# Optimization experiments

Hardware: AMD Instinct MI355X
Metric: run time of the kernel (lower is better)

## Reference

```python
import jax, jax.numpy as jnp
import numpy as np

B = 4096          # number of sampled constraints (batch)
H = 1024          # hidden_size
N_UNIT = 5
MAXD = 4          # max(DEPTHS)
TAU = 1.0
N_STEPS = N_UNIT * (1 + 2 * MAXD)  # 45
CLIST = np.linspace(10.0, 20.0, 5).astype(np.float32)
NSC = 11
DEPTH_VALS = np.array([2, 3, 4])
RATIO_VALS = np.array([3, 4, 6])
KS_VALS = np.array([3, 5, 7])


def setup_inputs() -> dict:
    key = jax.random.key(0)
    ks = jax.random.split(key, 20)
    def p(k, shape):
        return jax.random.uniform(k, shape, minval=-0.1, maxval=0.1, dtype=jnp.float32)
    return {
        'constraints': jax.random.uniform(ks[0], (B,), minval=10.0, maxval=20.0, dtype=jnp.float32),
        'superclass_id': 3,
        'gumbel_u': jax.random.uniform(ks[1], (N_STEPS, B, 3), minval=1e-6, maxval=1.0 - 1e-6, dtype=jnp.float32),
        'cond_emb': p(ks[2], (len(CLIST), H // 2)),
        'sc_emb': p(ks[3], (NSC, H // 2)),
        'depth_emb': p(ks[4], (3, H)),
        'ratio_emb': p(ks[5], (3, H)),
        'ks_emb': p(ks[6], (3, H)),
        'W_ih': p(ks[7], (4 * H, H)), 'b_ih': p(ks[8], (4 * H,)),
        'W_hh': p(ks[9], (4 * H, H)), 'b_hh': p(ks[10], (4 * H,)),
        'depth_W': p(ks[11], (3, H)), 'depth_b': p(ks[12], (3,)),
        'width_W': p(ks[13], (3, H)), 'width_b': p(ks[14], (3,)),
        'ks_W': p(ks[15], (3, H)), 'ks_b': p(ks[16], (3,)),
    }


def reference(constraints, superclass_id, gumbel_u, cond_emb, sc_emb, depth_emb, ratio_emb,
              ks_emb, W_ih, b_ih, W_hh, b_hh, depth_W, depth_b, width_W, width_b, ks_W, ks_b):
    clist = jnp.asarray(CLIST)
    # linear_interpolation: find bracketing interval for each constraint
    idx = jnp.clip(jnp.searchsorted(clist, constraints, side='right') - 1, 0, clist.shape[0] - 2)
    left, right = clist[idx], clist[idx + 1]
    w = ((right - constraints) / (right - left))[:, None]
    cemb = w * cond_emb[idx] + (1.0 - w) * cond_emb[idx + 1]          # [B, H/2]
    sce = jnp.broadcast_to(sc_emb[superclass_id], (constraints.shape[0], sc_emb.shape[1]))
    embed = jnp.concatenate([cemb, sce], axis=1)                       # [B, H]
    h = jnp.zeros((constraints.shape[0], H), embed.dtype)
    c = h

    def lstm(x, h, c):
        gates = x @ W_ih.T + b_ih + h @ W_hh.T + b_hh                  # [B, 4H]
        i, f, g, o = jnp.split(gates, 4, axis=-1)
        c2 = jax.nn.sigmoid(f) * c + jax.nn.sigmoid(i) * jnp.tanh(g)
        h2 = jax.nn.sigmoid(o) * jnp.tanh(c2)
        return h2, c2

    def gsample(logits, u):
        g = -jnp.log(-jnp.log(u))
        y_soft = jax.nn.softmax((logits + g) / TAU, axis=-1)
        onehot = jax.nn.one_hot(jnp.argmax(y_soft, -1), logits.shape[-1], dtype=y_soft.dtype)
        y_hard = onehot - jax.lax.stop_gradient(y_soft) + y_soft       # straight-through
        return jnp.argmax(y_hard, -1), y_soft, y_hard

    t = 0
    d_idx, d_probs, d_wbs = [], [], []
    r_idx, r_probs, r_wbs = [], [], []
    k_idx, k_probs, k_wbs = [], [], []
    for _unit in range(N_UNIT):
        h, c = lstm(embed, h, c)
        s, ys, yh = gsample(h @ depth_W.T + depth_b, gumbel_u[t]); t += 1
        d_idx.append(s); d_probs.append(ys); d_wbs.append(yh)
        embed = depth_emb[s]
        for _blk in range(MAXD):
            h, c = lstm(embed, h, c)
            s, ys, yh = gsample(h @ width_W.T + width_b, gumbel_u[t]); t += 1
            r_idx.append(s); r_probs.append(ys); r_wbs.append(yh)
            embed = ratio_emb[s]
            h, c = lstm(embed, h, c)
            s, ys, yh = gsample(h @ ks_W.T + ks_b, gumbel_u[t]); t += 1
            k_idx.append(s); k_probs.append(ys); k_wbs.append(yh)
            embed = ks_emb[s]

    depths = jnp.asarray(DEPTH_VALS)[jnp.stack(d_idx)]   # [5, B]
    ratios = jnp.asarray(RATIO_VALS)[jnp.stack(r_idx)]   # [20, B]
    kss = jnp.asarray(KS_VALS)[jnp.stack(k_idx)]         # [20, B]
    return (depths, ratios, kss,
            jnp.stack(d_wbs), jnp.stack(d_probs),
            jnp.stack(r_wbs), jnp.stack(r_probs),
            jnp.stack(k_wbs), jnp.stack(k_probs))
```

## Files before the change

### kernel.cpp

```cpp
#include <hip/hip_runtime.h>
#include <cmath>

namespace {

typedef _Float16 f16;
typedef f16 f16x8 __attribute__((ext_vector_type(8)));
typedef f16 f16x4 __attribute__((ext_vector_type(4)));
typedef float f32x4 __attribute__((ext_vector_type(4)));

constexpr int B  = 4096;
constexpr int H  = 1024;
constexpr int FH = 4 * H;
constexpr int NSTEPS = 45;
constexpr float INVS = 1.0f / 2048.0f;

__device__ __forceinline__ float sigf(float x) { return 1.0f / (1.0f + expf(-x)); }

struct HL { f16 h, l; };
__device__ __forceinline__ HL split16(float a) {
  float ah = (float)(f16)a;
  if (fabsf(a) < 6.1035156e-5f) ah = 0.0f;
  HL r; r.h = (f16)ah; r.l = (f16)((a - ah) * 2048.0f); return r;
}

__device__ __forceinline__ void async16(f16* lds_dst, const f16* gsrc) {
  __builtin_amdgcn_global_load_lds(
      (const __attribute__((address_space(1))) void*)gsrc,
      (__attribute__((address_space(3))) void*)lds_dst, 16, 0, 0);
}

__global__ void packW_kernel(const float* __restrict__ W, f16* __restrict__ packed) {
  int tid  = blockIdx.x * 256 + threadIdx.x;
  int lane = tid & 63;
  int rest = tid >> 6;
  int hl = rest & 1;
  int nf = (rest >> 1) & 3;
  int wn = (rest >> 3) & 1;
  int kt = (rest >> 4) & 31;
  int jb = rest >> 9;
  int row = nf * 1024 + jb * 32 + wn * 16 + (lane & 15);
  int kk  = kt * 32 + (lane >> 4) * 8;
  const float* src = W + (size_t)row * H + kk;
  f16x8 v;
  #pragma unroll
  for (int i = 0; i < 8; ++i) {
    HL s = split16(src[i]);
    v[i] = hl ? s.l : s.h;
  }
  *(f16x8*)(packed + (size_t)tid * 8) = v;
}

__global__ void precompute_kernel(
    const float* __restrict__ W_ih, const float* __restrict__ b_ih, const float* __restrict__ b_hh,
    const float* __restrict__ depth_emb, const float* __restrict__ ratio_emb, const float* __restrict__ ks_emb,
    const float* __restrict__ cond_emb, const float* __restrict__ sc_emb, const int* __restrict__ sid_p,
    float* __restrict__ tblD, float* __restrict__ tblR, float* __restrict__ tblK,
    float* __restrict__ condp, float* __restrict__ base0) {
  const int w4   = threadIdx.x >> 6;
  const int lane = threadIdx.x & 63;
  const int j    = blockIdx.x * 4 + w4;
  const float* wr = W_ih + (size_t)j * H;
  const int k = lane * 16;
  float4 wv0 = *(const float4*)(wr + k);
  float4 wv1 = *(const float4*)(wr + k + 4);
  float4 wv2 = *(const float4*)(wr + k + 8);
  float4 wv3 = *(const float4*)(wr + k + 12);

  auto dot = [&](const float* e) -> float {
    float4 e0 = *(const float4*)(e);
    float4 e1 = *(const float4*)(e + 4);
    float4 e2 = *(const float4*)(e + 8);
    float4 e3 = *(const float4*)(e + 12);
    return e0.x*wv0.x + e0.y*wv0.y + e0.z*wv0.z + e0.w*wv0.w
         + e1.x*wv1.x + e1.y*wv1.y + e1.z*wv1.z + e1.w*wv1.w
         + e2.x*wv2.x + e2.y*wv2.y + e2.z*wv2.z + e2.w*wv2.w
         + e3.x*wv3.x + e3.y*wv3.y + e3.z*wv3.z + e3.w*wv3.w;
  };

  float a[15];
  a[0] = dot(depth_emb + k);       a[1] = dot(depth_emb + H + k);   a[2] = dot(depth_emb + 2*H + k);
  a[3] = dot(ratio_emb + k);       a[4] = dot(ratio_emb + H + k);   a[5] = dot(ratio_emb + 2*H + k);
  a[6] = dot(ks_emb + k);          a[7] = dot(ks_emb + H + k);      a[8] = dot(ks_emb + 2*H + k);
  a[9] = a[10] = a[11] = a[12] = a[13] = a[14] = 0.0f;
  constexpr int HH = H / 2;
  int sid = sid_p[0];
  if (lane < 32) {
    a[9]  = dot(cond_emb + 0*HH + k);
    a[10] = dot(cond_emb + 1*HH + k);
    a[11] = dot(cond_emb + 2*HH + k);
    a[12] = dot(cond_emb + 3*HH + k);
    a[13] = dot(cond_emb + 4*HH + k);
  } else {
    a[14] = dot(sc_emb + sid*HH + (k - HH));
  }
  #pragma unroll
  for (int i = 0; i < 15; ++i) {
    #pragma unroll
    for (int off = 32; off > 0; off >>= 1) a[i] += __shfl_xor(a[i], off);
  }
  if (lane == 0) {
    float bias = b_ih[j] + b_hh[j];
    tblD[0*FH+j]=a[0]+bias; tblD[1*FH+j]=a[1]+bias; tblD[2*FH+j]=a[2]+bias;
    tblR[0*FH+j]=a[3]+bias; tblR[1*FH+j]=a[4]+bias; tblR[2*FH+j]=a[5]+bias;
    tblK[0*FH+j]=a[6]+bias; tblK[1*FH+j]=a[7]+bias; tblK[2*FH+j]=a[8]+bias;
    condp[0*FH+j]=a[9]; condp[1*FH+j]=a[10]; condp[2*FH+j]=a[11];
    condp[3*FH+j]=a[12]; condp[4*FH+j]=a[13];
    base0[j] = a[14] + bias;
  }
}

__global__ void step0_kernel(const float* __restrict__ constraints,
                             const float* __restrict__ condp, const float* __restrict__ base0,
                             f16* __restrict__ hhi, f16* __restrict__ hlo, float* __restrict__ c) {
  int idx = blockIdx.x * blockDim.x + threadIdx.x;
  int b = idx >> 10;
  int j = idx & (H - 1);
  float cv = constraints[b];
  int i0 = 0;
  if (cv >= 12.5f) i0 = 1;
  if (cv >= 15.0f) i0 = 2;
  if (cv >= 17.5f) i0 = 3;
  float right = 10.0f + 2.5f * (float)(i0 + 1);
  float w = (right - cv) / 2.5f;
  const float* c0 = condp + (size_t)i0 * FH;
  const float* c1 = c0 + FH;
  float iw = 1.0f - w;
  float xi = w*c0[j]       + iw*c1[j]       + base0[j];
  float xg = w*c0[2*H+j]   + iw*c1[2*H+j]   + base0[2*H+j];
  float xo = w*c0[3*H+j]   + iw*c1[3*H+j]   + base0[3*H+j];
  float cn = sigf(xi) * tanhf(xg);
  float hn = sigf(xo) * tanhf(cn);
  c[idx] = cn;
  HL s = split16(hn);
  hhi[idx] = s.h; hlo[idx] = s.l;
}

constexpr int ABUF = 16384;

__global__ __launch_bounds__(512, 2) void lstm_step_mfma(
    const f16* __restrict__ hhi, const f16* __restrict__ hlo,
    f16* __restrict__ nhhi, f16* __restrict__ nhlo,
    float* __restrict__ cbuf,
    const f16* __restrict__ packW,
    const float* __restrict__ tbl, const int* __restrict__ sel) {
  __shared__ __align__(16) f16 lds[3 * ABUF];

  const int tid  = threadIdx.x;
  const int lane = tid & 63;
  const int w    = tid >> 6;
  const int wm   = w >> 1, wn = w & 1;
  const int l15  = lane & 15;
  const int kq   = lane >> 4;

  const int L   = blockIdx.x;
  const int xcd = L & 7, seq = L >> 3;
  const int jb  = (xcd << 2) + (seq & 3);
  const int bb  = seq >> 2;
  const int b0  = bb << 8;
  const int j0  = jb << 5;

  f32x4 accH[4][4] = {};
  f32x4 accL[4][4] = {};

  int offA[4];
  #pragma unroll
  for (int mf = 0; mf < 4; ++mf) {
    int R = wm * 64 + mf * 16 + l15;
    int c = kq ^ (R & 3) ^ ((R >> 2) & 3);
    offA[mf] = R * 32 + c * 8;
  }

  const int rs = tid >> 2, cs = tid & 3;
  const int r1 = 128 + rs;
  const int cl0 = cs ^ (rs & 3) ^ ((rs >> 2) & 3);
  const int cl1 = cs ^ (r1 & 3) ^ ((r1 >> 2) & 3);
  const f16* sA0h = hhi + (size_t)(b0 + rs) * H + cl0 * 8;
  const f16* sA0l = hlo + (size_t)(b0 + rs) * H + cl0 * 8;
  const f16* sA1h = hhi + (size_t)(b0 + r1) * H + cl1 * 8;
  const f16* sA1l = hlo + (size_t)(b0 + r1) * H + cl1 * 8;
  const int dA0 = w * 512, dA1 = 4096 + w * 512;

  f16 *bA = lds, *bB = lds + ABUF, *bC = lds + 2 * ABUF;

  auto stageA = [&](f16* buf, int ko) {
    async16(buf + dA0,        sA0h + ko);
    async16(buf + dA0 + 8192, sA0l + ko);
    async16(buf + dA1,        sA1h + ko);
    async16(buf + dA1 + 8192, sA1l + ko);
  };

  const f16* wb = packW + (size_t)jb * 262144 + wn * 4096 + lane * 8;

  f16x8 bh0[4], bh1[4], bl[4];

  stageA(bA, 0);
  stageA(bB, 32);
  #pragma unroll
  for (int nf = 0; nf < 4; ++nf) bh0[nf] = *(const f16x8*)(wb + nf * 1024);
  asm volatile("s_waitcnt vmcnt(8)" ::: "memory");
  __builtin_amdgcn_s_barrier();

  auto tile = [&](int kt, f16x8 (&bhC)[4], f16x8 (&bhN)[4]) {
    const f16* wt = wb + (size_t)kt * 8192;
    #pragma unroll
    for (int nf = 0; nf < 4; ++nf) bl[nf] = *(const f16x8*)(wt + nf * 1024 + 512);
    if (kt < 30) stageA(bC, (kt + 2) * 32);
    if (kt < 31) {
      #pragma unroll
      for (int nf = 0; nf < 4; ++nf) bhN[nf] = *(const f16x8*)(wt + 8192 + nf * 1024);
    }
    f16x8 ah[4], al[4];
    #pragma unroll
    for (int mf = 0; mf < 4; ++mf) {
      ah[mf] = *(const f16x8*)(bA + offA[mf]);
      al[mf] = *(const f16x8*)(bA + offA[mf] + 8192);
    }
    #pragma unroll
    for (int mf = 0; mf < 4; ++mf)
      #pragma unroll
      for (int nf = 0; nf < 4; ++nf)
        accH[mf][nf] = __builtin_amdgcn_mfma_f32_16x16x32_f16(ah[mf], bhC[nf], accH[mf][nf], 0, 0, 0);
    #pragma unroll
    for (int mf = 0; mf < 4; ++mf)
      #pragma unroll
      for (int nf = 0; nf < 4; ++nf) {
        accL[mf][nf] = __builtin_amdgcn_mfma_f32_16x16x32_f16(ah[mf], bl[nf], accL[mf][nf], 0, 0, 0);
        accL[mf][nf] = __builtin_amdgcn_mfma_f32_16x16x32_f16(al[mf], bhC[nf], accL[mf][nf], 0, 0, 0);
      }
    __builtin_amdgcn_s_barrier();
    f16* tt = bA; bA = bB; bB = bC; bC = tt;
  };

  for (int kt = 0; kt < 32; kt += 2) {
    tile(kt,     bh0, bh1);
    tile(kt + 1, bh1, bh0);
  }

  const int j = j0 + wn * 16 + l15;
  #pragma unroll
  for (int mf = 0; mf < 4; ++mf) {
    #pragma unroll
    for (int r = 0; r < 4; ++r) {
      int b = b0 + wm * 64 + mf * 16 + kq * 4 + r;
      int s = sel[b];
      const float* tb = tbl + (size_t)s * FH + j;
      float gi = accH[mf][0][r] + accL[mf][0][r] * INVS + tb[0];
      float gf = accH[mf][1][r] + accL[mf][1][r] * INVS + tb[H];
      float gg = accH[mf][2][r] + accL[mf][2][r] * INVS + tb[2*H];
      float go = accH[mf][3][r] + accL[mf][3][r] * INVS + tb[3*H];
      size_t off = (size_t)b * H + j;
      float cp = cbuf[off];
      float cn = sigf(gf) * cp + sigf(gi) * tanhf(gg);
      float hn = sigf(go) * tanhf(cn);
      cbuf[off] = cn;
      HL sp = split16(hn);
      nhhi[off] = sp.h;
      nhlo[off] = sp.l;
    }
  }
}

__global__ void sampler_kernel(const f16* __restrict__ hhi, const f16* __restrict__ hlo,
                               const float* __restrict__ selW, const float* __restrict__ selb,
                               const float* __restrict__ gu,
                               float* __restrict__ val_out, float* __restrict__ wb_out,
                               float* __restrict__ p_out,
                               float v0, float v1, float v2,
                               int* __restrict__ sel) {
  int wave = threadIdx.x >> 6;
  int lane = threadIdx.x & 63;
  int b = blockIdx.x * 4 + wave;
  const f16* hh = hhi + (size_t)b * H;
  const f16* hl = hlo + (size_t)b * H;
  float acc0 = 0, acc1 = 0, acc2 = 0;
  #pragma unroll
  for (int ch = 0; ch < 4; ++ch) {
    int k = ch * 256 + lane * 4;
    f16x4 vh = *(const f16x4*)(hh + k);
    f16x4 vl = *(const f16x4*)(hl + k);
    float x0 = (float)vh[0] + (float)vl[0] * INVS;
    float x1 = (float)vh[1] + (float)vl[1] * INVS;
    float x2 = (float)vh[2] + (float)vl[2] * INVS;
    float x3 = (float)vh[3] + (float)vl[3] * INVS;
    float4 w0 = *(const float4*)(selW + k);
    float4 w1 = *(const float4*)(selW + H + k);
    float4 w2 = *(const float4*)(selW + 2*H + k);
    acc0 += x0*w0.x + x1*w0.y + x2*w0.z + x3*w0.w;
    acc1 += x0*w1.x + x1*w1.y + x2*w1.z + x3*w1.w;
    acc2 += x0*w2.x + x1*w2.y + x2*w2.z + x3*w2.w;
  }
  #pragma unroll
  for (int off = 32; off > 0; off >>= 1) {
    acc0 += __shfl_xor(acc0, off);
    acc1 += __shfl_xor(acc1, off);
    acc2 += __shfl_xor(acc2, off);
  }
  if (lane == 0) {
    float y0 = acc0 + selb[0] - logf(-logf(gu[(size_t)b*3 + 0]));
    float y1 = acc1 + selb[1] - logf(-logf(gu[(size_t)b*3 + 1]));
    float y2 = acc2 + selb[2] - logf(-logf(gu[(size_t)b*3 + 2]));
    int s = 0;
    float best = y0;
    if (y1 > best) { s = 1; best = y1; }
    if (y2 > best) { s = 2; best = y2; }
    float e0 = expf(y0 - best), e1 = expf(y1 - best), e2 = expf(y2 - best);
    float inv = 1.0f / (e0 + e1 + e2);
    float p0 = e0 * inv, p1 = e1 * inv, p2 = e2 * inv;
    val_out[b] = (s == 0) ? v0 : ((s == 1) ? v1 : v2);
    wb_out[(size_t)b*3 + 0] = (s == 0) ? 1.0f : 0.0f;
    wb_out[(size_t)b*3 + 1] = (s == 1) ? 1.0f : 0.0f;
    wb_out[(size_t)b*3 + 2] = (s == 2) ? 1.0f : 0.0f;
    p_out[(size_t)b*3 + 0] = p0;
    p_out[(size_t)b*3 + 1] = p1;
    p_out[(size_t)b*3 + 2] = p2;
    sel[b] = s;
  }
}

}

extern "C" void kernel_launch(void* const* d_in, const int* in_sizes, int n_in,
                              void* d_out, int out_size, void* d_ws, size_t ws_size,
                              hipStream_t stream) {
  (void)in_sizes; (void)n_in; (void)out_size; (void)ws_size;
  const float* constraints = (const float*)d_in[0];
  const int*   sid         = (const int*)d_in[1];
  const float* gumbel      = (const float*)d_in[2];
  const float* cond_emb    = (const float*)d_in[3];
  const float* sc_emb      = (const float*)d_in[4];
  const float* depth_emb   = (const float*)d_in[5];
  const float* ratio_emb   = (const float*)d_in[6];
  const float* ks_emb      = (const float*)d_in[7];
  const float* W_ih        = (const float*)d_in[8];
  const float* b_ih        = (const float*)d_in[9];
  const float* W_hh        = (const float*)d_in[10];
  const float* b_hh        = (const float*)d_in[11];
  const float* depth_W     = (const float*)d_in[12];
  const float* depth_b     = (const float*)d_in[13];
  const float* width_W     = (const float*)d_in[14];
  const float* width_b     = (const float*)d_in[15];
  const float* ks_W        = (const float*)d_in[16];
  const float* ks_b        = (const float*)d_in[17];

  float* out = (float*)d_out;
  float* ws  = (float*)d_ws;

  float* cb    = ws;
  f16*   packW = (f16*)(cb + (size_t)B * H);
  f16*   hhiA  = packW + (size_t)8 * 1024 * 1024;
  f16*   hloA  = hhiA + (size_t)B * H;
  f16*   hhiB  = hloA + (size_t)B * H;
  f16*   hloB  = hhiB + (size_t)B * H;
  float* tblD  = (float*)(hloB + (size_t)B * H);
  float* tblR  = tblD + 3 * FH;
  float* tblK  = tblR + 3 * FH;
  float* condp = tblK + 3 * FH;
  float* base0 = condp + 5 * FH;
  int*   sel   = (int*)(base0 + FH);

  packW_kernel<<<4096, 256, 0, stream>>>(W_hh, packW);
  precompute_kernel<<<FH / 4, 256, 0, stream>>>(
      W_ih, b_ih, b_hh, depth_emb, ratio_emb, ks_emb, cond_emb, sc_emb, sid,
      tblD, tblR, tblK, condp, base0);
  step0_kernel<<<(B * H) / 256, 256, 0, stream>>>(constraints, condp, base0, hhiA, hloA, cb);

  const float* selW_arr[3] = {depth_W, width_W, ks_W};
  const float* selb_arr[3] = {depth_b, width_b, ks_b};
  const float vals[3][3]   = {{2.f,3.f,4.f},{3.f,4.f,6.f},{3.f,5.f,7.f}};
  float* tbl_arr[3]        = {tblD, tblR, tblK};

  const size_t DEPTHS = 0,            RATIOS = (size_t)5*B,   KSS    = (size_t)25*B,
               DWBS   = (size_t)45*B, DPROBS = (size_t)60*B,
               RWBS   = (size_t)75*B, RPROBS = (size_t)135*B,
               KWBS   = (size_t)195*B, KPROBS = (size_t)255*B;

  f16* hhi_cur = hhiA; f16* hlo_cur = hloA;
  f16* hhi_nxt = hhiB; f16* hlo_nxt = hloB;
  for (int t = 0; t < NSTEPS; ++t) {
    if (t > 0) {
      int pt = (t - 1) % 9;
      int ptype = (pt == 0) ? 0 : ((pt & 1) ? 1 : 2);
      lstm_step_mfma<<<512, 512, 0, stream>>>(
          hhi_cur, hlo_cur, hhi_nxt, hlo_nxt, cb, packW, tbl_arr[ptype], sel);
      f16* th = hhi_cur; hhi_cur = hhi_nxt; hhi_nxt = th;
      f16* tl = hlo_cur; hlo_cur = hlo_nxt; hlo_nxt = tl;
    }
    int r = t % 9, u = t / 9;
    int ty, row;
    float *valp, *wbp, *pp;
    if (r == 0)      { ty = 0; row = u;
      valp = out + DEPTHS + (size_t)row*B; wbp = out + DWBS + (size_t)row*B*3; pp = out + DPROBS + (size_t)row*B*3; }
    else if (r & 1)  { ty = 1; row = u*4 + (r-1)/2;
      valp = out + RATIOS + (size_t)row*B; wbp = out + RWBS + (size_t)row*B*3; pp = out + RPROBS + (size_t)row*B*3; }
    else             { ty = 2; row = u*4 + (r-2)/2;
      valp = out + KSS + (size_t)row*B;    wbp = out + KWBS + (size_t)row*B*3; pp = out + KPROBS + (size_t)row*B*3; }
    sampler_kernel<<<B / 4, 256, 0, stream>>>(
        hhi_cur, hlo_cur, selW_arr[ty], selb_arr[ty], gumbel + (size_t)t * B * 3,
        valp, wbp, pp, vals[ty][0], vals[ty][1], vals[ty][2], sel);
  }
}
```

Before: 5.705 ms.

## Store hidden state in MFMA-fragment packed layout and load A directly from global

The hi/lo split hidden state now lives in one buffer laid out in MFMA A-fragment order. The LSTM step kernel drops its LDS triple-buffered async staging and barriers, and each wave reads its A fragments straight from global memory (mostly L2) while double-buffering the W fragments in registers. The step0 kernel, the step epilogue and the sampler are changed to write and read this packed layout. Launch bounds move to one block per CU, which trades occupancy for register room, and every wave now refetches A from global with no LDS reuse across the two column waves.

```diff
diff --git a/kernel.cpp b/kernel.cpp
--- a/kernel.cpp
+++ b/kernel.cpp
@@ -23,11 +23,6 @@
   HL r; r.h = (f16)ah; r.l = (f16)((a - ah) * 2048.0f); return r;
 }
 
-__device__ __forceinline__ void async16(f16* lds_dst, const f16* gsrc) {
-  __builtin_amdgcn_global_load_lds(
-      (const __attribute__((address_space(1))) void*)gsrc,
-      (__attribute__((address_space(3))) void*)lds_dst, 16, 0, 0);
-}
 
 __global__ void packW_kernel(const float* __restrict__ W, f16* __restrict__ packed) {
   int tid  = blockIdx.x * 256 + threadIdx.x;
@@ -111,7 +106,7 @@
 
 __global__ void step0_kernel(const float* __restrict__ constraints,
                              const float* __restrict__ condp, const float* __restrict__ base0,
-                             f16* __restrict__ hhi, f16* __restrict__ hlo, float* __restrict__ c) {
+                             f16* __restrict__ hpack, float* __restrict__ c) {
   int idx = blockIdx.x * blockDim.x + threadIdx.x;
   int b = idx >> 10;
   int j = idx & (H - 1);
@@ -132,19 +127,17 @@
   float hn = sigf(xo) * tanhf(cn);
   c[idx] = cn;
   HL s = split16(hn);
-  hhi[idx] = s.h; hlo[idx] = s.l;
-}
-
-constexpr int ABUF = 16384;
-
-__global__ __launch_bounds__(512, 2) void lstm_step_mfma(
-    const f16* __restrict__ hhi, const f16* __restrict__ hlo,
-    f16* __restrict__ nhhi, f16* __restrict__ nhlo,
+  size_t u = (size_t)((b >> 4) * 32 + (j >> 5));
+  int off = ((b & 15) + 16 * ((j >> 3) & 3)) * 8 + (j & 7);
+  hpack[u * 1024 + off]       = s.h;
+  hpack[u * 1024 + off + 512] = s.l;
+}
+
+__global__ __launch_bounds__(512, 1) void lstm_step_mfma(
+    const f16* __restrict__ hpack, f16* __restrict__ npack,
     float* __restrict__ cbuf,
     const f16* __restrict__ packW,
     const float* __restrict__ tbl, const int* __restrict__ sel) {
-  __shared__ __align__(16) f16 lds[3 * ABUF];
-
   const int tid  = threadIdx.x;
   const int lane = tid & 63;
   const int w    = tid >> 6;
@@ -162,58 +155,35 @@
   f32x4 accH[4][4] = {};
   f32x4 accL[4][4] = {};
 
-  int offA[4];
-  #pragma unroll
-  for (int mf = 0; mf < 4; ++mf) {
-    int R = wm * 64 + mf * 16 + l15;
-    int c = kq ^ (R & 3) ^ ((R >> 2) & 3);
-    offA[mf] = R * 32 + c * 8;
-  }
-
-  const int rs = tid >> 2, cs = tid & 3;
-  const int r1 = 128 + rs;
-  const int cl0 = cs ^ (rs & 3) ^ ((rs >> 2) & 3);
-  const int cl1 = cs ^ (r1 & 3) ^ ((r1 >> 2) & 3);
-  const f16* sA0h = hhi + (size_t)(b0 + rs) * H + cl0 * 8;
-  const f16* sA0l = hlo + (size_t)(b0 + rs) * H + cl0 * 8;
-  const f16* sA1h = hhi + (size_t)(b0 + r1) * H + cl1 * 8;
-  const f16* sA1l = hlo + (size_t)(b0 + r1) * H + cl1 * 8;
-  const int dA0 = w * 512, dA1 = 4096 + w * 512;
-
-  f16 *bA = lds, *bB = lds + ABUF, *bC = lds + 2 * ABUF;
-
-  auto stageA = [&](f16* buf, int ko) {
-    async16(buf + dA0,        sA0h + ko);
-    async16(buf + dA0 + 8192, sA0l + ko);
-    async16(buf + dA1,        sA1h + ko);
-    async16(buf + dA1 + 8192, sA1l + ko);
-  };
+  const f16* abase[4];
+  #pragma unroll
+  for (int mf = 0; mf < 4; ++mf)
+    abase[mf] = hpack + ((size_t)((b0 >> 4) + wm * 4 + mf) * 32) * 1024 + lane * 8;
 
   const f16* wb = packW + (size_t)jb * 262144 + wn * 4096 + lane * 8;
 
-  f16x8 bh0[4], bh1[4], bl[4];
-
-  stageA(bA, 0);
-  stageA(bB, 32);
-  #pragma unroll
-  for (int nf = 0; nf < 4; ++nf) bh0[nf] = *(const f16x8*)(wb + nf * 1024);
-  asm volatile("s_waitcnt vmcnt(8)" ::: "memory");
-  __builtin_amdgcn_s_barrier();
-
-  auto tile = [&](int kt, f16x8 (&bhC)[4], f16x8 (&bhN)[4]) {
-    const f16* wt = wb + (size_t)kt * 8192;
-    #pragma unroll
-    for (int nf = 0; nf < 4; ++nf) bl[nf] = *(const f16x8*)(wt + nf * 1024 + 512);
-    if (kt < 30) stageA(bC, (kt + 2) * 32);
+  f16x8 bhX[4], blX[4], bhY[4], blY[4];
+
+  #pragma unroll
+  for (int nf = 0; nf < 4; ++nf) {
+    bhX[nf] = *(const f16x8*)(wb + nf * 1024);
+    blX[nf] = *(const f16x8*)(wb + nf * 1024 + 512);
+  }
+
+  auto tile = [&](int kt, f16x8 (&bhC)[4], f16x8 (&blC)[4],
+                          f16x8 (&bhN)[4], f16x8 (&blN)[4]) {
+    f16x8 ah[4], al[4];
+    #pragma unroll
+    for (int mf = 0; mf < 4; ++mf) ah[mf] = *(const f16x8*)(abase[mf] + kt * 1024);
+    #pragma unroll
+    for (int mf = 0; mf < 4; ++mf) al[mf] = *(const f16x8*)(abase[mf] + kt * 1024 + 512);
     if (kt < 31) {
+      const f16* wt = wb + (size_t)(kt + 1) * 8192;
       #pragma unroll
-      for (int nf = 0; nf < 4; ++nf) bhN[nf] = *(const f16x8*)(wt + 8192 + nf * 1024);
-    }
-    f16x8 ah[4], al[4];
-    #pragma unroll
-    for (int mf = 0; mf < 4; ++mf) {
-      ah[mf] = *(const f16x8*)(bA + offA[mf]);
-      al[mf] = *(const f16x8*)(bA + offA[mf] + 8192);
+      for (int nf = 0; nf < 4; ++nf) {
+        bhN[nf] = *(const f16x8*)(wt + nf * 1024);
+        blN[nf] = *(const f16x8*)(wt + nf * 1024 + 512);
+      }
     }
     #pragma unroll
     for (int mf = 0; mf < 4; ++mf)
@@ -223,22 +193,25 @@
     #pragma unroll
     for (int mf = 0; mf < 4; ++mf)
       #pragma unroll
-      for (int nf = 0; nf < 4; ++nf) {
-        accL[mf][nf] = __builtin_amdgcn_mfma_f32_16x16x32_f16(ah[mf], bl[nf], accL[mf][nf], 0, 0, 0);
+      for (int nf = 0; nf < 4; ++nf)
+        accL[mf][nf] = __builtin_amdgcn_mfma_f32_16x16x32_f16(ah[mf], blC[nf], accL[mf][nf], 0, 0, 0);
+    #pragma unroll
+    for (int mf = 0; mf < 4; ++mf)
+      #pragma unroll
+      for (int nf = 0; nf < 4; ++nf)
         accL[mf][nf] = __builtin_amdgcn_mfma_f32_16x16x32_f16(al[mf], bhC[nf], accL[mf][nf], 0, 0, 0);
-      }
-    __builtin_amdgcn_s_barrier();
-    f16* tt = bA; bA = bB; bB = bC; bC = tt;
   };
 
   for (int kt = 0; kt < 32; kt += 2) {
-    tile(kt,     bh0, bh1);
-    tile(kt + 1, bh1, bh0);
+    tile(kt,     bhX, blX, bhY, blY);
+    tile(kt + 1, bhY, blY, bhX, blX);
   }
 
   const int j = j0 + wn * 16 + l15;
+  const int eoff = (wn * 2 + (l15 >> 3)) * 128 + (l15 & 7);
   #pragma unroll
   for (int mf = 0; mf < 4; ++mf) {
+    const size_t ubase = ((size_t)((b0 >> 4) + wm * 4 + mf) * 32 + jb) * 1024;
     #pragma unroll
     for (int r = 0; r < 4; ++r) {
       int b = b0 + wm * 64 + mf * 16 + kq * 4 + r;
@@ -254,13 +227,14 @@
       float hn = sigf(go) * tanhf(cn);
       cbuf[off] = cn;
       HL sp = split16(hn);
-      nhhi[off] = sp.h;
-      nhlo[off] = sp.l;
+      size_t pa = ubase + (size_t)((kq * 4 + r) * 8 + eoff);
+      npack[pa]       = sp.h;
+      npack[pa + 512] = sp.l;
     }
   }
 }
 
-__global__ void sampler_kernel(const f16* __restrict__ hhi, const f16* __restrict__ hlo,
+__global__ void sampler_kernel(const f16* __restrict__ hpack,
                                const float* __restrict__ selW, const float* __restrict__ selb,
                                const float* __restrict__ gu,
                                float* __restrict__ val_out, float* __restrict__ wb_out,
@@ -270,24 +244,25 @@
   int wave = threadIdx.x >> 6;
   int lane = threadIdx.x & 63;
   int b = blockIdx.x * 4 + wave;
-  const f16* hh = hhi + (size_t)b * H;
-  const f16* hl = hlo + (size_t)b * H;
+  const f16* hp = hpack + ((size_t)(b >> 4) * 32) * 1024 + (b & 15) * 8;
   float acc0 = 0, acc1 = 0, acc2 = 0;
   #pragma unroll
-  for (int ch = 0; ch < 4; ++ch) {
-    int k = ch * 256 + lane * 4;
-    f16x4 vh = *(const f16x4*)(hh + k);
-    f16x4 vl = *(const f16x4*)(hl + k);
-    float x0 = (float)vh[0] + (float)vl[0] * INVS;
-    float x1 = (float)vh[1] + (float)vl[1] * INVS;
-    float x2 = (float)vh[2] + (float)vl[2] * INVS;
-    float x3 = (float)vh[3] + (float)vl[3] * INVS;
-    float4 w0 = *(const float4*)(selW + k);
-    float4 w1 = *(const float4*)(selW + H + k);
-    float4 w2 = *(const float4*)(selW + 2*H + k);
-    acc0 += x0*w0.x + x1*w0.y + x2*w0.z + x3*w0.w;
-    acc1 += x0*w1.x + x1*w1.y + x2*w1.z + x3*w1.w;
-    acc2 += x0*w2.x + x1*w2.y + x2*w2.z + x3*w2.w;
+  for (int c2 = 0; c2 < 2; ++c2) {
+    int c = lane + c2 * 64;
+    const f16* base = hp + (c >> 2) * 1024 + (c & 3) * 128;
+    f16x8 vh = *(const f16x8*)(base);
+    f16x8 vl = *(const f16x8*)(base + 512);
+    int j = c * 8;
+    const float* w0p = selW + j;
+    const float* w1p = selW + H + j;
+    const float* w2p = selW + 2 * H + j;
+    #pragma unroll
+    for (int i = 0; i < 8; ++i) {
+      float x = (float)vh[i] + (float)vl[i] * INVS;
+      acc0 += x * w0p[i];
+      acc1 += x * w1p[i];
+      acc2 += x * w2p[i];
+    }
   }
   #pragma unroll
   for (int off = 32; off > 0; off >>= 1) {
@@ -347,11 +322,9 @@
 
   float* cb    = ws;
   f16*   packW = (f16*)(cb + (size_t)B * H);
-  f16*   hhiA  = packW + (size_t)8 * 1024 * 1024;
-  f16*   hloA  = hhiA + (size_t)B * H;
-  f16*   hhiB  = hloA + (size_t)B * H;
-  f16*   hloB  = hhiB + (size_t)B * H;
-  float* tblD  = (float*)(hloB + (size_t)B * H);
+  f16*   hpkA  = packW + (size_t)8 * 1024 * 1024;
+  f16*   hpkB  = hpkA + (size_t)B * H * 2;
+  float* tblD  = (float*)(hpkB + (size_t)B * H * 2);
   float* tblR  = tblD + 3 * FH;
   float* tblK  = tblR + 3 * FH;
   float* condp = tblK + 3 * FH;
@@ -362,7 +335,7 @@
   precompute_kernel<<<FH / 4, 256, 0, stream>>>(
       W_ih, b_ih, b_hh, depth_emb, ratio_emb, ks_emb, cond_emb, sc_emb, sid,
       tblD, tblR, tblK, condp, base0);
-  step0_kernel<<<(B * H) / 256, 256, 0, stream>>>(constraints, condp, base0, hhiA, hloA, cb);
+  step0_kernel<<<(B * H) / 256, 256, 0, stream>>>(constraints, condp, base0, hpkA, cb);
 
   const float* selW_arr[3] = {depth_W, width_W, ks_W};
   const float* selb_arr[3] = {depth_b, width_b, ks_b};
@@ -374,16 +347,15 @@
                RWBS   = (size_t)75*B, RPROBS = (size_t)135*B,
                KWBS   = (size_t)195*B, KPROBS = (size_t)255*B;
 
-  f16* hhi_cur = hhiA; f16* hlo_cur = hloA;
-  f16* hhi_nxt = hhiB; f16* hlo_nxt = hloB;
+  f16* hcur = hpkA;
+  f16* hnxt = hpkB;
   for (int t = 0; t < NSTEPS; ++t) {
     if (t > 0) {
       int pt = (t - 1) % 9;
       int ptype = (pt == 0) ? 0 : ((pt & 1) ? 1 : 2);
       lstm_step_mfma<<<512, 512, 0, stream>>>(
-          hhi_cur, hlo_cur, hhi_nxt, hlo_nxt, cb, packW, tbl_arr[ptype], sel);
-      f16* th = hhi_cur; hhi_cur = hhi_nxt; hhi_nxt = th;
-      f16* tl = hlo_cur; hlo_cur = hlo_nxt; hlo_nxt = tl;
+          hcur, hnxt, cb, packW, tbl_arr[ptype], sel);
+      f16* tmp = hcur; hcur = hnxt; hnxt = tmp;
     }
     int r = t % 9, u = t / 9;
     int ty, row;
@@ -395,7 +367,7 @@
     else             { ty = 2; row = u*4 + (r-2)/2;
       valp = out + KSS + (size_t)row*B;    wbp = out + KWBS + (size_t)row*B*3; pp = out + KPROBS + (size_t)row*B*3; }
     sampler_kernel<<<B / 4, 256, 0, stream>>>(
-        hhi_cur, hlo_cur, selW_arr[ty], selb_arr[ty], gumbel + (size_t)t * B * 3,
+        hcur, selW_arr[ty], selb_arr[ty], gumbel + (size_t)t * B * 3,
         valp, wbp, pp, vals[ty][0], vals[ty][1], vals[ty][2], sel);
   }
 }
```

Result: faster. 5.382 ms (-5.7%).
